# Kernel optimization log

Hardware: AMD Instinct MI355X
Metric: run time of the kernel (lower is better)

Reference implementation:

```python
import jax, jax.numpy as jnp
import numpy as np

DIM = 32  # fixed internal node dim
N_GRAPHS = 64


def setup_inputs() -> dict:
    key = jax.random.key(0)
    ks = jax.random.split(key, 16)
    N, E, F_N, F_E, H = 12500, 200000, 16, 8, 32
    inp = {
        "x": jax.random.normal(ks[0], (N, F_N), dtype=jnp.float32),
        "edge_index": jax.random.randint(ks[1], (2, E), 0, N, dtype=jnp.int64),
        "edge_attr": jax.random.normal(ks[2], (E, F_E), dtype=jnp.float32),
        "batch": jnp.sort(jax.random.randint(ks[3], (N,), 0, N_GRAPHS, dtype=jnp.int64)),
        "lin0_w": jax.random.normal(ks[4], (DIM, F_N), dtype=jnp.float32) * 0.1,
        "lin0_b": jax.random.normal(ks[5], (DIM,), dtype=jnp.float32) * 0.1,
        "nn_w": jax.random.normal(ks[6], (DIM * H, F_E), dtype=jnp.float32) * 0.1,
        "nn_b": jax.random.normal(ks[7], (DIM * H,), dtype=jnp.float32) * 0.1,
        "root_w": jax.random.normal(ks[8], (DIM, H), dtype=jnp.float32) * 0.1,
        "conv_b": jax.random.normal(ks[9], (H,), dtype=jnp.float32) * 0.1,
        "lin1_w": jax.random.normal(ks[10], (16, H), dtype=jnp.float32) * 0.1,
        "lin1_b": jax.random.normal(ks[11], (16,), dtype=jnp.float32) * 0.1,
        "lin2_w": jax.random.normal(ks[12], (1, 16), dtype=jnp.float32) * 0.1,
        "lin2_b": jax.random.normal(ks[13], (1,), dtype=jnp.float32) * 0.1,
    }
    return inp


def reference(x, edge_index, edge_attr, batch, lin0_w, lin0_b, nn_w, nn_b,
              root_w, conv_b, lin1_w, lin1_b, lin2_w, lin2_b):
    N = x.shape[0]
    H = conv_b.shape[0]
    # lin0 + relu -> node features [N, DIM]
    out = jax.nn.relu(x @ lin0_w.T + lin0_b)
    # NNConv: per-edge weight matrices from edge MLP (single Linear)
    src, dst = edge_index[0], edge_index[1]
    w_e = (edge_attr @ nn_w.T + nn_b).reshape(-1, DIM, H)  # [E, DIM, H]
    msg = jnp.einsum('ed,edh->eh', out[src], w_e)          # gather + per-edge matmul
    agg = jax.ops.segment_sum(msg, dst, num_segments=N)     # scatter-add
    h = jax.nn.relu(agg + out @ root_w + conv_b)             # root weight + bias
    # global add pool over graphs
    u = jax.ops.segment_sum(h, batch, num_segments=N_GRAPHS)  # [G, H]
    o = jax.nn.relu(u @ lin1_w.T + lin1_b)
    o = o @ lin2_w.T + lin2_b
    return o.reshape(-1)
```

## Files before the change

### kernel.cpp

```cpp
#include <hip/hip_runtime.h>

#define DIMN 32
#define HD   32
#define FN   16
#define FE   8
#define NG   64
#define CAP  64
#define K3T  512
#define K3W  (K3T / 64)

__global__ __launch_bounds__(256) void k1_out(
    const float* __restrict__ x, const float* __restrict__ lin0_w,
    const float* __restrict__ lin0_b,
    float* __restrict__ outn, float* __restrict__ aggfb, float* __restrict__ u,
    int* __restrict__ deg, int N)
{
    const int gt = blockIdx.x * 256 + threadIdx.x;
    if (gt >= N * DIMN) return;
    const int n = gt >> 5, d = gt & 31;

    float s = lin0_b[d];
    const float* xr = x + (size_t)n * FN;
    const float* wr = lin0_w + d * FN;
    #pragma unroll
    for (int j = 0; j < FN; ++j) s = fmaf(xr[j], wr[j], s);
    outn[gt] = fmaxf(s, 0.f);

    aggfb[gt] = 0.f;
    if (d == 0) deg[n] = 0;
    if (gt < NG * HD) u[gt] = 0.f;
}

__global__ __launch_bounds__(256) void kb_bucket(
    const int* __restrict__ ei, const float* __restrict__ ea,
    const float* __restrict__ outn, const float* __restrict__ nn_w,
    const float* __restrict__ nn_b,
    int* __restrict__ deg, int2* __restrict__ es, float* __restrict__ aggfb, int E)
{
    const int e = blockIdx.x * 256 + threadIdx.x;
    if (e >= E) return;
    const int src = ei[e];
    const int dst = ei[E + e];
    const int pos = atomicAdd(&deg[dst], 1);
    if (pos < CAP) {
        es[(size_t)dst * CAP + pos] = make_int2(e, src);
    } else {
        float ef[FE];
        #pragma unroll
        for (int f = 0; f < FE; ++f) ef[f] = ea[(size_t)e * FE + f];
        for (int h = 0; h < HD; ++h) {
            float m = 0.f;
            for (int d = 0; d < DIMN; ++d) {
                float wdh = nn_b[d * HD + h];
                #pragma unroll
                for (int f = 0; f < FE; ++f)
                    wdh = fmaf(ef[f], nn_w[(d * HD + h) * FE + f], wdh);
                m = fmaf(outn[(size_t)src * DIMN + d], wdh, m);
            }
            atomicAdd(aggfb + (size_t)dst * HD + h, m);
        }
    }
}

#define EDGE_FMA(o, a) \
    S  = (S + (o));                      \
    T0 = fmaf((o), (a).x, T0);           \
    T1 = fmaf((o), (a).y, T1);           \
    T2 = fmaf((o), (a).z, T2);           \
    T3 = fmaf((o), (a).w, T3);

#define CONTRIB(DD, A) { \
    const int d_ = d0 + (DD); \
    const float4 ta_ = *(const float4*)&s_T[w * 256 + d_ * 8]; \
    const float4 tb_ = *(const float4*)&s_T[w * 256 + d_ * 8 + 4]; \
    const float2 so_ = s_SO[w * 32 + d_]; \
    const int b_ = d_ * 256 + h; \
    A = fmaf(ta_.x, s_nnw2[b_      ], A); \
    A = fmaf(ta_.y, s_nnw2[b_ +  32], A); \
    A = fmaf(ta_.z, s_nnw2[b_ +  64], A); \
    A = fmaf(ta_.w, s_nnw2[b_ +  96], A); \
    A = fmaf(tb_.x, s_nnw2[b_ + 128], A); \
    A = fmaf(tb_.y, s_nnw2[b_ + 160], A); \
    A = fmaf(tb_.z, s_nnw2[b_ + 192], A); \
    A = fmaf(tb_.w, s_nnw2[b_ + 224], A); \
    A = fmaf(so_.x, s_nnb[d_ * 32 + h], A); \
    A = fmaf(so_.y, s_rw [d_ * 32 + h], A); }

__global__ __launch_bounds__(K3T, 6) void k3_gather(
    const float* __restrict__ ea, const float* __restrict__ outn,
    const int2* __restrict__ es, const float* __restrict__ nn_w,
    const float* __restrict__ nn_b, const float* __restrict__ root_w,
    const float* __restrict__ conv_b, const int* __restrict__ deg,
    const float* __restrict__ aggfb, const int* __restrict__ batch,
    float* __restrict__ u, int N)
{
    __shared__ float  s_nnw2[DIMN * FE * HD];
    __shared__ float  s_nnb[DIMN * HD];
    __shared__ float  s_rw[DIMN * HD];
    __shared__ float  s_cb[HD];
    __shared__ float  s_T[K3W * 256];
    __shared__ float2 s_SO[K3W * 32];
    __shared__ float  s_V[K3W * 32];
    __shared__ int    s_G[K3W];

    const int tid = threadIdx.x;
    for (int i = tid; i < DIMN * FE * HD; i += K3T) {
        const int d = i >> 8, f = (i >> 5) & 7, hh = i & 31;
        s_nnw2[i] = nn_w[d * 256 + hh * 8 + f];
    }
    for (int i = tid; i < DIMN * HD; i += K3T) { s_nnb[i] = nn_b[i]; s_rw[i] = root_w[i]; }
    if (tid < HD) s_cb[tid] = conv_b[tid];
    __syncthreads();

    const int l = tid & 63;
    const int h = l & 31;
    const int p = l >> 5;
    const int w = tid >> 6;
    const int n = blockIdx.x * K3W + w;

    int gval = -1;
    if (n < N) {
        const int nu = __builtin_amdgcn_readfirstlane(n);
        const int dn = min(deg[nu], CAP);
        const int2* ep = es + (size_t)nu * CAP;
        const int f0 = 4 * p;

        float T0 = 0.f, T1 = 0.f, T2 = 0.f, T3 = 0.f, S = 0.f;

        for (int j0 = 0; j0 < dn; j0 += 8) {
            const int jm = dn - 1;
            const int2 E0 = ep[j0];
            const int2 E1 = ep[min(j0 + 1, jm)];
            const int2 E2 = ep[min(j0 + 2, jm)];
            const int2 E3 = ep[min(j0 + 3, jm)];
            const int2 E4 = ep[min(j0 + 4, jm)];
            const int2 E5 = ep[min(j0 + 5, jm)];
            const int2 E6 = ep[min(j0 + 6, jm)];
            const int2 E7 = ep[min(j0 + 7, jm)];

            const float4 a0 = *(const float4*)(ea + (size_t)E0.x * FE + f0);
            const float4 a1 = *(const float4*)(ea + (size_t)E1.x * FE + f0);
            const float4 a2 = *(const float4*)(ea + (size_t)E2.x * FE + f0);
            const float4 a3 = *(const float4*)(ea + (size_t)E3.x * FE + f0);
            const float4 a4 = *(const float4*)(ea + (size_t)E4.x * FE + f0);
            const float4 a5 = *(const float4*)(ea + (size_t)E5.x * FE + f0);
            const float4 a6 = *(const float4*)(ea + (size_t)E6.x * FE + f0);
            const float4 a7 = *(const float4*)(ea + (size_t)E7.x * FE + f0);
            float o0 = outn[(size_t)E0.y * DIMN + h];
            float o1 = outn[(size_t)E1.y * DIMN + h];
            float o2 = outn[(size_t)E2.y * DIMN + h];
            float o3 = outn[(size_t)E3.y * DIMN + h];
            float o4 = outn[(size_t)E4.y * DIMN + h];
            float o5 = outn[(size_t)E5.y * DIMN + h];
            float o6 = outn[(size_t)E6.y * DIMN + h];
            float o7 = outn[(size_t)E7.y * DIMN + h];

            o1 = (j0 + 1 <= jm) ? o1 : 0.f;
            o2 = (j0 + 2 <= jm) ? o2 : 0.f;
            o3 = (j0 + 3 <= jm) ? o3 : 0.f;
            o4 = (j0 + 4 <= jm) ? o4 : 0.f;
            o5 = (j0 + 5 <= jm) ? o5 : 0.f;
            o6 = (j0 + 6 <= jm) ? o6 : 0.f;
            o7 = (j0 + 7 <= jm) ? o7 : 0.f;

            EDGE_FMA(o0, a0) EDGE_FMA(o1, a1) EDGE_FMA(o2, a2) EDGE_FMA(o3, a3)
            EDGE_FMA(o4, a4) EDGE_FMA(o5, a5) EDGE_FMA(o6, a6) EDGE_FMA(o7, a7)
        }

        *(float4*)&s_T[w * 256 + h * 8 + f0] = make_float4(T0, T1, T2, T3);
        if (p == 0) s_SO[w * 32 + h] = make_float2(S, outn[(size_t)nu * DIMN + h]);

        const float base = aggfb[(size_t)nu * HD + h] + s_cb[h];

        float acc0 = 0.f, acc1 = 0.f, acc2 = 0.f, acc3 = 0.f;
        const int d0 = p << 4;
        #pragma unroll
        for (int dd = 0; dd < 16; dd += 4) {
            CONTRIB(dd + 0, acc0)
            CONTRIB(dd + 1, acc1)
            CONTRIB(dd + 2, acc2)
            CONTRIB(dd + 3, acc3)
        }
        float acc = (acc0 + acc1) + (acc2 + acc3);
        acc += __shfl_xor(acc, 32);

        const float v = fmaxf(acc + base, 0.f);
        if (p == 0) s_V[w * 32 + h] = v;
        gval = batch[nu];
    }
    if (l == 0) s_G[w] = gval;
    __syncthreads();

    if (tid < 32) {
        float accp = 0.f;
        int   gc   = -1;
        #pragma unroll
        for (int ww = 0; ww < K3W; ++ww) {
            const int gg = s_G[ww];
            if (gg >= 0) {
                const float vv = s_V[ww * 32 + tid];
                if (gg != gc) {
                    if (gc >= 0) atomicAdd(u + (size_t)gc * HD + tid, accp);
                    gc = gg;
                    accp = vv;
                } else {
                    accp += vv;
                }
            }
        }
        if (gc >= 0) atomicAdd(u + (size_t)gc * HD + tid, accp);
    }
}

__global__ __launch_bounds__(64) void k4_head(
    const float* __restrict__ u, const float* __restrict__ lin1_w,
    const float* __restrict__ lin1_b, const float* __restrict__ lin2_w,
    const float* __restrict__ lin2_b, float* __restrict__ outp)
{
    const int g = threadIdx.x;
    if (g >= NG) return;

    float ur[HD];
    #pragma unroll
    for (int hh = 0; hh < HD; ++hh) ur[hh] = u[(size_t)g * HD + hh];

    float acc = lin2_b[0];
    #pragma unroll
    for (int i = 0; i < 16; ++i) {
        float o = lin1_b[i];
        #pragma unroll
        for (int hh = 0; hh < HD; ++hh)
            o = fmaf(ur[hh], lin1_w[i * HD + hh], o);
        o = fmaxf(o, 0.f);
        acc = fmaf(o, lin2_w[i], acc);
    }
    outp[g] = acc;
}

extern "C" void kernel_launch(void* const* d_in, const int* in_sizes, int n_in,
                              void* d_out, int out_size, void* d_ws, size_t ws_size,
                              hipStream_t stream)
{
    const float* x      = (const float*)d_in[0];
    const int*   ei     = (const int*)  d_in[1];
    const float* ea     = (const float*)d_in[2];
    const int*   batch  = (const int*)  d_in[3];
    const float* lin0_w = (const float*)d_in[4];
    const float* lin0_b = (const float*)d_in[5];
    const float* nn_w   = (const float*)d_in[6];
    const float* nn_b   = (const float*)d_in[7];
    const float* root_w = (const float*)d_in[8];
    const float* conv_b = (const float*)d_in[9];
    const float* lin1_w = (const float*)d_in[10];
    const float* lin1_b = (const float*)d_in[11];
    const float* lin2_w = (const float*)d_in[12];
    const float* lin2_b = (const float*)d_in[13];

    const int N = in_sizes[0] / FN;
    const int E = in_sizes[2] / FE;

    float* ws    = (float*)d_ws;
    float* outn  = ws;
    float* aggfb = outn  + (size_t)N * DIMN;
    float* u     = aggfb + (size_t)N * DIMN;
    int*   deg   = (int*)(u + (size_t)NG * HD);
    int2*  es    = (int2*)(deg + N);

    const int nb1 = (N * DIMN + 255) / 256;
    k1_out<<<nb1, 256, 0, stream>>>(x, lin0_w, lin0_b, outn, aggfb, u, deg, N);

    const int nbb = (E + 255) / 256;
    kb_bucket<<<nbb, 256, 0, stream>>>(ei, ea, outn, nn_w, nn_b, deg, es, aggfb, E);

    const int nb3 = (N + K3W - 1) / K3W;
    k3_gather<<<nb3, K3T, 0, stream>>>(ea, outn, es, nn_w, nn_b, root_w, conv_b,
                                       deg, aggfb, batch, u, N);

    k4_head<<<1, 64, 0, stream>>>(u, lin1_w, lin1_b, lin2_w, lin2_b, (float*)d_out);
}
```

Baseline: 160.2 us.

## Copy edge attributes into destination-bucketed buffer during bucketing

The bucketing kernel now reads each edge's 8 attributes coalesced and writes them into a per-destination slot buffer next to a separate source-index array. The gather kernel then reads edge attributes contiguously per node instead of through a dependent indirect load via the edge id. This removes one level of pointer chasing and the random gather of edge attributes in the gather kernel. In exchange the bucketing kernel writes more bytes (32 B per edge) and the workspace grows by N*CAP*8 floats.

Result: no change. 158.9 us (-0.8%).

```diff
diff --git a/kernel.cpp b/kernel.cpp
--- a/kernel.cpp
+++ b/kernel.cpp
@@ -35,19 +35,24 @@
     const int* __restrict__ ei, const float* __restrict__ ea,
     const float* __restrict__ outn, const float* __restrict__ nn_w,
     const float* __restrict__ nn_b,
-    int* __restrict__ deg, int2* __restrict__ es, float* __restrict__ aggfb, int E)
+    int* __restrict__ deg, int* __restrict__ esrc, float* __restrict__ eaB,
+    float* __restrict__ aggfb, int E)
 {
     const int e = blockIdx.x * 256 + threadIdx.x;
     if (e >= E) return;
     const int src = ei[e];
     const int dst = ei[E + e];
+    const float4 w0 = *(const float4*)(ea + (size_t)e * FE);
+    const float4 w1 = *(const float4*)(ea + (size_t)e * FE + 4);
     const int pos = atomicAdd(&deg[dst], 1);
     if (pos < CAP) {
-        es[(size_t)dst * CAP + pos] = make_int2(e, src);
+        const size_t slot = (size_t)dst * CAP + pos;
+        esrc[slot] = src;
+        float4* eb = (float4*)(eaB + slot * 8);
+        eb[0] = w0;
+        eb[1] = w1;
     } else {
-        float ef[FE];
-        #pragma unroll
-        for (int f = 0; f < FE; ++f) ef[f] = ea[(size_t)e * FE + f];
+        const float ef[FE] = {w0.x, w0.y, w0.z, w0.w, w1.x, w1.y, w1.z, w1.w};
         for (int h = 0; h < HD; ++h) {
             float m = 0.f;
             for (int d = 0; d < DIMN; ++d) {
@@ -87,8 +92,8 @@
     A = fmaf(so_.y, s_rw [d_ * 32 + h], A); }
 
 __global__ __launch_bounds__(K3T, 6) void k3_gather(
-    const float* __restrict__ ea, const float* __restrict__ outn,
-    const int2* __restrict__ es, const float* __restrict__ nn_w,
+    const float* __restrict__ eaB, const float* __restrict__ outn,
+    const int* __restrict__ esrc, const float* __restrict__ nn_w,
     const float* __restrict__ nn_b, const float* __restrict__ root_w,
     const float* __restrict__ conv_b, const int* __restrict__ deg,
     const float* __restrict__ aggfb, const int* __restrict__ batch,
@@ -122,38 +127,38 @@
     if (n < N) {
         const int nu = __builtin_amdgcn_readfirstlane(n);
         const int dn = min(deg[nu], CAP);
-        const int2* ep = es + (size_t)nu * CAP;
+        const int*   sp = esrc + (size_t)nu * CAP;
+        const float* eb = eaB  + (size_t)nu * CAP * 8;
         const int f0 = 4 * p;
 
         float T0 = 0.f, T1 = 0.f, T2 = 0.f, T3 = 0.f, S = 0.f;
 
+        const int jm = dn - 1;
         for (int j0 = 0; j0 < dn; j0 += 8) {
-            const int jm = dn - 1;
-            const int2 E0 = ep[j0];
-            const int2 E1 = ep[min(j0 + 1, jm)];
-            const int2 E2 = ep[min(j0 + 2, jm)];
-            const int2 E3 = ep[min(j0 + 3, jm)];
-            const int2 E4 = ep[min(j0 + 4, jm)];
-            const int2 E5 = ep[min(j0 + 5, jm)];
-            const int2 E6 = ep[min(j0 + 6, jm)];
-            const int2 E7 = ep[min(j0 + 7, jm)];
-
-            const float4 a0 = *(const float4*)(ea + (size_t)E0.x * FE + f0);
-            const float4 a1 = *(const float4*)(ea + (size_t)E1.x * FE + f0);
-            const float4 a2 = *(const float4*)(ea + (size_t)E2.x * FE + f0);
-            const float4 a3 = *(const float4*)(ea + (size_t)E3.x * FE + f0);
-            const float4 a4 = *(const float4*)(ea + (size_t)E4.x * FE + f0);
-            const float4 a5 = *(const float4*)(ea + (size_t)E5.x * FE + f0);
-            const float4 a6 = *(const float4*)(ea + (size_t)E6.x * FE + f0);
-            const float4 a7 = *(const float4*)(ea + (size_t)E7.x * FE + f0);
-            float o0 = outn[(size_t)E0.y * DIMN + h];
-            float o1 = outn[(size_t)E1.y * DIMN + h];
-            float o2 = outn[(size_t)E2.y * DIMN + h];
-            float o3 = outn[(size_t)E3.y * DIMN + h];
-            float o4 = outn[(size_t)E4.y * DIMN + h];
-            float o5 = outn[(size_t)E5.y * DIMN + h];
-            float o6 = outn[(size_t)E6.y * DIMN + h];
-            float o7 = outn[(size_t)E7.y * DIMN + h];
+            const int j1 = min(j0 + 1, jm), j2 = min(j0 + 2, jm);
+            const int j3 = min(j0 + 3, jm), j4 = min(j0 + 4, jm);
+            const int j5 = min(j0 + 5, jm), j6 = min(j0 + 6, jm);
+            const int j7 = min(j0 + 7, jm);
+
+            const float4 a0 = *(const float4*)(eb + (size_t)j0 * 8 + f0);
+            const float4 a1 = *(const float4*)(eb + (size_t)j1 * 8 + f0);
+            const float4 a2 = *(const float4*)(eb + (size_t)j2 * 8 + f0);
+            const float4 a3 = *(const float4*)(eb + (size_t)j3 * 8 + f0);
+            const float4 a4 = *(const float4*)(eb + (size_t)j4 * 8 + f0);
+            const float4 a5 = *(const float4*)(eb + (size_t)j5 * 8 + f0);
+            const float4 a6 = *(const float4*)(eb + (size_t)j6 * 8 + f0);
+            const float4 a7 = *(const float4*)(eb + (size_t)j7 * 8 + f0);
+
+            const int s0 = sp[j0], s1 = sp[j1], s2 = sp[j2], s3 = sp[j3];
+            const int s4 = sp[j4], s5 = sp[j5], s6 = sp[j6], s7 = sp[j7];
+            float o0 = outn[(size_t)s0 * DIMN + h];
+            float o1 = outn[(size_t)s1 * DIMN + h];
+            float o2 = outn[(size_t)s2 * DIMN + h];
+            float o3 = outn[(size_t)s3 * DIMN + h];
+            float o4 = outn[(size_t)s4 * DIMN + h];
+            float o5 = outn[(size_t)s5 * DIMN + h];
+            float o6 = outn[(size_t)s6 * DIMN + h];
+            float o7 = outn[(size_t)s7 * DIMN + h];
 
             o1 = (j0 + 1 <= jm) ? o1 : 0.f;
             o2 = (j0 + 2 <= jm) ? o2 : 0.f;
@@ -260,20 +265,22 @@
     const int E = in_sizes[2] / FE;
 
     float* ws    = (float*)d_ws;
-    float* outn  = ws;
-    float* aggfb = outn  + (size_t)N * DIMN;
+    float* eaB   = ws;
+    float* outn  = eaB  + (size_t)N * CAP * 8;
+    float* aggfb = outn + (size_t)N * DIMN;
     float* u     = aggfb + (size_t)N * DIMN;
     int*   deg   = (int*)(u + (size_t)NG * HD);
-    int2*  es    = (int2*)(deg + N);
+    int*   esrc  = deg + N;
 
     const int nb1 = (N * DIMN + 255) / 256;
     k1_out<<<nb1, 256, 0, stream>>>(x, lin0_w, lin0_b, outn, aggfb, u, deg, N);
 
     const int nbb = (E + 255) / 256;
-    kb_bucket<<<nbb, 256, 0, stream>>>(ei, ea, outn, nn_w, nn_b, deg, es, aggfb, E);
+    kb_bucket<<<nbb, 256, 0, stream>>>(ei, ea, outn, nn_w, nn_b, deg, esrc, eaB,
+                                       aggfb, E);
 
     const int nb3 = (N + K3W - 1) / K3W;
-    k3_gather<<<nb3, K3T, 0, stream>>>(ea, outn, es, nn_w, nn_b, root_w, conv_b,
+    k3_gather<<<nb3, K3T, 0, stream>>>(eaB, outn, esrc, nn_w, nn_b, root_w, conv_b,
                                        deg, aggfb, batch, u, N);
 
     k4_head<<<1, 64, 0, stream>>>(u, lin1_w, lin1_b, lin2_w, lin2_b, (float*)d_out);
```
